# Kernel optimization log

Measured on AMD Instinct MI355X. Metric: run time of the kernel, lower is better.

## Reference

```python
import jax, jax.numpy as jnp
import numpy as np

B, S, D, H, BS = 4, 4096, 1024, 16, 256
DH = D // H  # 64
NB = S // BS  # 16 blocks


def setup_inputs() -> dict:
    key = jax.random.key(0)
    ks = jax.random.split(key, 16)
    sc = 1.0 / np.sqrt(D).astype(np.float32)

    def lin(k):
        return jax.random.normal(k, (D, D), jnp.float32) * sc

    zb = jnp.zeros((D,), jnp.float32)
    return {
        "x": jax.random.normal(ks[0], (B, S, D), jnp.float32),
        "lq_w": lin(ks[1]), "lq_b": zb,
        "lk_w": lin(ks[2]), "lk_b": zb,
        "lv_w": lin(ks[3]), "lv_b": zb,
        "lo_w": lin(ks[4]), "lo_b": zb,
        "pos_bias": jax.random.normal(ks[5], (1, H, BS, BS), jnp.float32) * 0.1,
        "sq_w": lin(ks[6]), "sq_b": zb,
        "sk_w": lin(ks[7]), "sk_b": zb,
        "sv_w": lin(ks[8]), "sv_b": zb,
        "so_w": lin(ks[9]), "so_b": zb,
        "sum_w": lin(ks[10]), "sum_b": zb,
    }


def _mha(x, qw, qb, kw, kb, vw, vb, ow, ob, bias=None):
    # x: [N, L, D] -> multi-head attention, optional additive position bias.
    N, L, _ = x.shape
    q = (x @ qw + qb).reshape(N, L, H, DH).transpose(0, 2, 1, 3)  # [N,H,L,DH]
    k = (x @ kw + kb).reshape(N, L, H, DH).transpose(0, 2, 1, 3)
    v = (x @ vw + vb).reshape(N, L, H, DH).transpose(0, 2, 1, 3)
    scores = jnp.einsum("nhqd,nhkd->nhqk", q, k) / jnp.sqrt(jnp.float32(DH))
    if bias is not None:
        scores = scores + bias[:, :, :L, :L]
    w = jax.nn.softmax(scores, axis=-1)
    ctx = jnp.einsum("nhqk,nhkd->nhqd", w, v)
    ctx = ctx.transpose(0, 2, 1, 3).reshape(N, L, D)
    return ctx @ ow + ob


def reference(x, lq_w, lq_b, lk_w, lk_b, lv_w, lv_b, lo_w, lo_b, pos_bias,
              sq_w, sq_b, sk_w, sk_b, sv_w, sv_b, so_w, so_b, sum_w, sum_b):
    # Local block attention with learned position bias (seq already multiple of BS)
    xb = x.reshape(B * NB, BS, D)
    local = _mha(xb, lq_w, lq_b, lk_w, lk_b, lv_w, lv_b, lo_w, lo_b,
                 bias=pos_bias).reshape(B, S, D)
    # Block summaries: mean-pool each block then linear summarizer
    summaries = x.reshape(B, NB, BS, D).mean(axis=2) @ sum_w + sum_b  # [B,NB,D]
    # Global attention over block summaries (no position bias)
    summ = _mha(summaries, sq_w, sq_b, sk_w, sk_b, sv_w, sv_b, so_w, so_b)
    # Broadcast each block's summary context back to its tokens and combine
    summ_exp = jnp.repeat(summ, BS, axis=1)  # [B,S,D]
    return local + summ_exp
```

## Files before the change

### kernel.cpp

```cpp
#include <hip/hip_runtime.h>
#include <hip/hip_bf16.h>

typedef unsigned short u16;
typedef __bf16 bf16x8 __attribute__((ext_vector_type(8)));
typedef float floatx4 __attribute__((ext_vector_type(4)));
typedef unsigned short u16x4 __attribute__((ext_vector_type(4)));
typedef unsigned short u16x8 __attribute__((ext_vector_type(8)));

__device__ __forceinline__ float b2f(u16 v) {
  unsigned u = ((unsigned)v) << 16;
  return __builtin_bit_cast(float, u);
}
__device__ __forceinline__ u16 f2b(float f) {
  unsigned u = __builtin_bit_cast(unsigned, f);
  unsigned r = (u + 0x7FFFu + ((u >> 16) & 1u)) >> 16;
  return (u16)r;
}
__device__ __forceinline__ void cp16(const u16* g, u16* l) {
  __builtin_amdgcn_global_load_lds(
      (const __attribute__((address_space(1))) unsigned int*)g,
      (__attribute__((address_space(3))) unsigned int*)l, 16, 0, 0);
}

struct GemmArgs {
  const u16* A;
  const u16* BT0; const u16* BT1; const u16* BT2;
  const float* b0; const float* b1; const float* b2;
  const float* summ;
  int srow0;
  u16* C0; u16* C1; u16* C2;
  float* Cf;
};

__global__ __launch_bounds__(256, 2) void gemm_bt(GemmArgs g) {
  const int z = blockIdx.z;
  const u16* A      = g.A;
  const u16* BT     = (z == 0) ? g.BT0 : (z == 1 ? g.BT1 : g.BT2);
  const float* bias = (z == 0) ? g.b0  : (z == 1 ? g.b1  : g.b2);
  u16* C            = (z == 0) ? g.C0  : (z == 1 ? g.C1  : g.C2);

  __shared__ u16 As[128 * 32];
  __shared__ u16 Bs[128 * 32];

  const int tid  = threadIdx.x;
  const int lane = tid & 63;
  const int wave = tid >> 6;
  const int quad = lane >> 4;
  const int cl   = lane & 15;
  const int wm   = wave & 1;
  const int wn   = wave >> 1;

  const size_t row0 = (size_t)blockIdx.x * 128;
  const size_t col0 = (size_t)blockIdx.y * 128;

  const int srow = lane >> 2;
  const int soff = (lane & 3) << 3;

  const u16* gA0 = A + (row0 + (size_t)(wave * 16 + srow)) * 1024 + soff;
  const u16* gA1 = gA0 + (size_t)64 * 1024;
  const u16* gB0 = BT + (col0 + (size_t)(wave * 16 + srow)) * 1024 + soff;
  const u16* gB1 = gB0 + (size_t)64 * 1024;
  u16* lA0 = As + wave * 512 + lane * 8;
  u16* lA1 = lA0 + 2048;
  u16* lB0 = Bs + wave * 512 + lane * 8;
  u16* lB1 = lB0 + 2048;

  floatx4 acc[4][4] = {};

  for (int kt = 0; kt < 1024; kt += 32) {
    __syncthreads();
    cp16(gA0, lA0); cp16(gA1, lA1);
    cp16(gB0, lB0); cp16(gB1, lB1);
    gA0 += 32; gA1 += 32; gB0 += 32; gB1 += 32;
    __syncthreads();
    bf16x8 af[4], bfr[4];
#pragma unroll
    for (int m = 0; m < 4; ++m)
      af[m] = *(const bf16x8*)&As[(wm * 64 + m * 16 + cl) * 32 + quad * 8];
#pragma unroll
    for (int n = 0; n < 4; ++n)
      bfr[n] = *(const bf16x8*)&Bs[(wn * 64 + n * 16 + cl) * 32 + quad * 8];
#pragma unroll
    for (int m = 0; m < 4; ++m)
#pragma unroll
      for (int n = 0; n < 4; ++n)
        acc[m][n] = __builtin_amdgcn_mfma_f32_16x16x32_bf16(af[m], bfr[n],
                                                            acc[m][n], 0, 0, 0);
  }

  const float* summ = g.summ;
#pragma unroll
  for (int m = 0; m < 4; ++m) {
    const size_t rbase = row0 + wm * 64 + m * 16 + quad * 4;
#pragma unroll
    for (int n = 0; n < 4; ++n) {
      const size_t c = col0 + wn * 64 + n * 16 + cl;
      const float bb = bias[c];
#pragma unroll
      for (int e = 0; e < 4; ++e) {
        float v = acc[m][n][e] + bb;
        if (summ)
          v += summ[(size_t)((int)((rbase + e) >> 8) + g.srow0) * 1024 + c];
        if (g.Cf) g.Cf[(rbase + e) * 1024 + c] = v;
        else      C[(rbase + e) * 1024 + c] = f2b(v);
      }
    }
  }
}

__global__ __launch_bounds__(256, 2) void local_attn(
    const u16* __restrict__ Q, const u16* __restrict__ Kt,
    const u16* __restrict__ Vt, const float* __restrict__ pbias,
    u16* __restrict__ ctx) {
  const int qt  = blockIdx.x;
  const int h   = blockIdx.y;
  const int blk = blockIdx.z;
  const int tid  = threadIdx.x;
  const int lane = tid & 63;
  const int w    = tid >> 6;
  const int quad = lane >> 4;
  const int cl   = lane & 15;

  __shared__ u16 BufA[64 * 72];
  __shared__ u16 BufB[64 * 72];

  const size_t tok0  = (size_t)blk * 256;
  const size_t qrow0 = tok0 + qt * 64;
  const int hc = h * 64;

  for (int i = tid; i < 512; i += 256) {
    const int row = i >> 3, c8 = (i & 7) * 8;
    *(u16x8*)&BufA[row * 72 + c8] =
        *(const u16x8*)&Q[(qrow0 + row) * 1024 + hc + c8];
  }

  floatx4 accS[16] = {};
#pragma unroll
  for (int kc = 0; kc < 4; ++kc) {
    __syncthreads();
    for (int i = tid; i < 512; i += 256) {
      const int row = i >> 3, c8 = (i & 7) * 8;
      *(u16x8*)&BufB[row * 72 + c8] =
          *(const u16x8*)&Kt[(tok0 + kc * 64 + row) * 1024 + hc + c8];
    }
    __syncthreads();
#pragma unroll
    for (int ki = 0; ki < 2; ++ki) {
      const bf16x8 aq =
          *(const bf16x8*)&BufA[(w * 16 + cl) * 72 + ki * 32 + quad * 8];
#pragma unroll
      for (int n = 0; n < 4; ++n) {
        const bf16x8 bk =
            *(const bf16x8*)&BufB[(n * 16 + cl) * 72 + ki * 32 + quad * 8];
        accS[kc * 4 + n] = __builtin_amdgcn_mfma_f32_16x16x32_bf16(
            aq, bk, accS[kc * 4 + n], 0, 0, 0);
      }
    }
  }

  float mrow[4] = {-1e30f, -1e30f, -1e30f, -1e30f};
#pragma unroll
  for (int r = 0; r < 4; ++r) {
    const float* brow = pbias + ((size_t)h << 16) +
                        (size_t)(qt * 64 + w * 16 + quad * 4 + r) * 256 + cl;
#pragma unroll
    for (int n = 0; n < 16; ++n) {
      float s = accS[n][r] * 0.125f + brow[n * 16];
      accS[n][r] = s;
      mrow[r] = fmaxf(mrow[r], s);
    }
  }
#pragma unroll
  for (int r = 0; r < 4; ++r) {
#pragma unroll
    for (int st = 1; st < 16; st <<= 1)
      mrow[r] = fmaxf(mrow[r], __shfl_xor(mrow[r], st));
  }
  float lsum[4] = {0.f, 0.f, 0.f, 0.f};
#pragma unroll
  for (int n = 0; n < 16; ++n) {
#pragma unroll
    for (int r = 0; r < 4; ++r) {
      float p = exp2f((accS[n][r] - mrow[r]) * 1.44269504f);
      accS[n][r] = p;
      lsum[r] += p;
    }
  }
#pragma unroll
  for (int r = 0; r < 4; ++r) {
#pragma unroll
    for (int st = 1; st < 16; st <<= 1)
      lsum[r] += __shfl_xor(lsum[r], st);
  }

  floatx4 accO[4] = {};
#pragma unroll
  for (int kc = 0; kc < 4; ++kc) {
    __syncthreads();
#pragma unroll
    for (int nn = 0; nn < 4; ++nn)
#pragma unroll
      for (int r = 0; r < 4; ++r)
        BufA[(w * 16 + quad * 4 + r) * 72 + nn * 16 + cl] =
            f2b(accS[kc * 4 + nn][r]);
    for (int i = tid; i < 512; i += 256) {
      const int key = i & 63, dh0 = (i >> 6) * 8;
      u16x8 v = *(const u16x8*)&Vt[(tok0 + kc * 64 + key) * 1024 + hc + dh0];
#pragma unroll
      for (int j = 0; j < 8; ++j) BufB[(dh0 + j) * 72 + key] = v[j];
    }
    __syncthreads();
#pragma unroll
    for (int ki = 0; ki < 2; ++ki) {
      const bf16x8 ap =
          *(const bf16x8*)&BufA[(w * 16 + cl) * 72 + ki * 32 + quad * 8];
#pragma unroll
      for (int nd = 0; nd < 4; ++nd) {
        const bf16x8 bv =
            *(const bf16x8*)&BufB[(nd * 16 + cl) * 72 + ki * 32 + quad * 8];
        accO[nd] = __builtin_amdgcn_mfma_f32_16x16x32_bf16(ap, bv, accO[nd],
                                                           0, 0, 0);
      }
    }
  }

  float inv[4];
#pragma unroll
  for (int r = 0; r < 4; ++r) inv[r] = 1.0f / lsum[r];
#pragma unroll
  for (int nd = 0; nd < 4; ++nd)
#pragma unroll
    for (int r = 0; r < 4; ++r)
      ctx[(qrow0 + w * 16 + quad * 4 + r) * 1024 + hc + nd * 16 + cl] =
          f2b(accO[nd][r] * inv[r]);
}

__global__ void cvt_x(const float* __restrict__ x, u16* __restrict__ xb) {
  const size_t i = ((size_t)blockIdx.x * 256 + threadIdx.x) * 4;
  float4 v = *(const float4*)&x[i];
  u16x4 o;
  o[0] = f2b(v.x); o[1] = f2b(v.y); o[2] = f2b(v.z); o[3] = f2b(v.w);
  *(u16x4*)&xb[i] = o;
}

__global__ void block_mean(const float* __restrict__ x, u16* __restrict__ xm) {
  const int g = blockIdx.x >> 2;
  const int d = ((blockIdx.x & 3) << 8) + threadIdx.x;
  const float* p = x + (size_t)g * 256 * 1024 + d;
  float s = 0.f;
  for (int t = 0; t < 256; ++t) s += p[(size_t)t * 1024];
  xm[(size_t)g * 1024 + d] = f2b(s * (1.0f / 256.0f));
}

__global__ void summ_attn(const u16* __restrict__ SQ, const u16* __restrict__ SK,
                          const u16* __restrict__ SV, u16* __restrict__ sctx) {
  const int b = blockIdx.x >> 4;
  const int h = blockIdx.x & 15;
  const int t = threadIdx.x;
  __shared__ float Qf[16][64];
  __shared__ float Kf[16][64];
  __shared__ float Vf[16][64];
  __shared__ float sc[16][16];
  for (int i = t; i < 1024; i += 64) {
    const int r = i >> 6, d = i & 63;
    const size_t off = (size_t)(b * 16 + r) * 1024 + h * 64 + d;
    Qf[r][d] = b2f(SQ[off]);
    Kf[r][d] = b2f(SK[off]);
    Vf[r][d] = b2f(SV[off]);
  }
  __syncthreads();
  {
    const int i = t >> 2, j0 = t & 3;
#pragma unroll
    for (int jj = 0; jj < 4; ++jj) {
      const int j = j0 + jj * 4;
      float s = 0.f;
      for (int d = 0; d < 64; ++d) s += Qf[i][d] * Kf[j][d];
      sc[i][j] = s * 0.125f;
    }
  }
  __syncthreads();
  if (t < 16) {
    float m = -1e30f;
    for (int j = 0; j < 16; ++j) m = fmaxf(m, sc[t][j]);
    float l = 0.f;
    for (int j = 0; j < 16; ++j) {
      float p = exp2f((sc[t][j] - m) * 1.44269504f);
      sc[t][j] = p;
      l += p;
    }
    const float inv = 1.0f / l;
    for (int j = 0; j < 16; ++j) sc[t][j] *= inv;
  }
  __syncthreads();
  {
    const int i = t >> 2, d0 = (t & 3) * 16;
    for (int dd = 0; dd < 16; ++dd) {
      float a = 0.f;
      for (int j = 0; j < 16; ++j) a += sc[i][j] * Vf[j][d0 + dd];
      sctx[(size_t)(b * 16 + i) * 1024 + h * 64 + d0 + dd] = f2b(a);
    }
  }
}

struct TPtrs { const float* src[9]; u16* dst[9]; };

__global__ void cvt_transpose9(TPtrs p) {
  const float* src = p.src[blockIdx.z];
  u16* dst         = p.dst[blockIdx.z];
  __shared__ u16 tile[64][72];
  const int r0 = blockIdx.x * 64, c0 = blockIdx.y * 64;
  for (int i = threadIdx.x; i < 1024; i += 256) {
    const int row = i >> 4, c4 = (i & 15) * 4;
    float4 v = *(const float4*)&src[(size_t)(r0 + row) * 1024 + c0 + c4];
    tile[row][c4 + 0] = f2b(v.x);
    tile[row][c4 + 1] = f2b(v.y);
    tile[row][c4 + 2] = f2b(v.z);
    tile[row][c4 + 3] = f2b(v.w);
  }
  __syncthreads();
  for (int i = threadIdx.x; i < 512; i += 256) {
    const int row = i >> 3, c8 = (i & 7) * 8;
    u16x8 v;
#pragma unroll
    for (int j = 0; j < 8; ++j) v[j] = tile[c8 + j][row];
    *(u16x8*)&dst[(size_t)(c0 + row) * 1024 + r0 + c8] = v;
  }
}

extern "C" void kernel_launch(void* const* d_in, const int* in_sizes, int n_in,
                              void* d_out, int out_size, void* d_ws, size_t ws_size,
                              hipStream_t stream) {
  const float* x    = (const float*)d_in[0];
  const float* lqw  = (const float*)d_in[1];
  const float* lqb  = (const float*)d_in[2];
  const float* lkw  = (const float*)d_in[3];
  const float* lkb  = (const float*)d_in[4];
  const float* lvw  = (const float*)d_in[5];
  const float* lvb  = (const float*)d_in[6];
  const float* low_ = (const float*)d_in[7];
  const float* lob  = (const float*)d_in[8];
  const float* pb   = (const float*)d_in[9];
  const float* sqw  = (const float*)d_in[10];
  const float* sqb  = (const float*)d_in[11];
  const float* skw  = (const float*)d_in[12];
  const float* skb  = (const float*)d_in[13];
  const float* svw  = (const float*)d_in[14];
  const float* svb  = (const float*)d_in[15];
  const float* sow  = (const float*)d_in[16];
  const float* sob  = (const float*)d_in[17];
  const float* smw  = (const float*)d_in[18];
  const float* smb  = (const float*)d_in[19];

  char* W = (char*)d_ws;
  size_t off = 0;
  u16* wt[9];
  for (int i = 0; i < 9; ++i) { wt[i] = (u16*)(W + off); off += (size_t)1024 * 1024 * 2; }
  u16* Xb  = (u16*)(W + off); off += (size_t)16384 * 1024 * 2;
  u16* XM  = (u16*)(W + off); off += (size_t)128 * 1024 * 2;
  u16* SMR = (u16*)(W + off); off += (size_t)128 * 1024 * 2;
  u16* SQp = (u16*)(W + off); off += (size_t)128 * 1024 * 2;
  u16* SKp = (u16*)(W + off); off += (size_t)128 * 1024 * 2;
  u16* SVp = (u16*)(W + off); off += (size_t)128 * 1024 * 2;
  u16* SCT = (u16*)(W + off); off += (size_t)128 * 1024 * 2;
  float* SMM = (float*)(W + off); off += (size_t)128 * 1024 * 4;
  const size_t fixedB = off;

  int CH = 256;
  for (int c = 16384; c >= 256; c >>= 1) {
    if (fixedB + (size_t)4 * c * 1024 * 2 <= ws_size) { CH = c; break; }
  }
  u16* Qb  = (u16*)(W + fixedB);
  u16* Kb  = Qb + (size_t)CH * 1024;
  u16* Vb  = Kb + (size_t)CH * 1024;
  u16* CTX = Vb + (size_t)CH * 1024;

  TPtrs tp;
  tp.src[0] = lqw; tp.src[1] = lkw; tp.src[2] = lvw; tp.src[3] = low_;
  tp.src[4] = sqw; tp.src[5] = skw; tp.src[6] = svw; tp.src[7] = sow;
  tp.src[8] = smw;
  for (int i = 0; i < 9; ++i) tp.dst[i] = wt[i];
  cvt_transpose9<<<dim3(16, 16, 9), 256, 0, stream>>>(tp);

  cvt_x<<<dim3(16384), 256, 0, stream>>>(x, Xb);
  block_mean<<<dim3(256), 256, 0, stream>>>(x, XM);

  GemmArgs g1{};
  g1.A = XM; g1.BT0 = g1.BT1 = g1.BT2 = wt[8];
  g1.b0 = g1.b1 = g1.b2 = smb; g1.summ = nullptr; g1.srow0 = 0;
  g1.C0 = g1.C1 = g1.C2 = SMR; g1.Cf = nullptr;
  gemm_bt<<<dim3(1, 8, 1), 256, 0, stream>>>(g1);

  GemmArgs g2{};
  g2.A = SMR; g2.BT0 = wt[4]; g2.BT1 = wt[5]; g2.BT2 = wt[6];
  g2.b0 = sqb; g2.b1 = skb; g2.b2 = svb; g2.summ = nullptr; g2.srow0 = 0;
  g2.C0 = SQp; g2.C1 = SKp; g2.C2 = SVp; g2.Cf = nullptr;
  gemm_bt<<<dim3(1, 8, 3), 256, 0, stream>>>(g2);

  summ_attn<<<dim3(64), 64, 0, stream>>>(SQp, SKp, SVp, SCT);

  GemmArgs g3{};
  g3.A = SCT; g3.BT0 = g3.BT1 = g3.BT2 = wt[7];
  g3.b0 = g3.b1 = g3.b2 = sob; g3.summ = nullptr; g3.srow0 = 0;
  g3.C0 = g3.C1 = g3.C2 = nullptr; g3.Cf = SMM;
  gemm_bt<<<dim3(1, 8, 1), 256, 0, stream>>>(g3);

  for (int base = 0; base < 16384; base += CH) {
    GemmArgs g4{};
    g4.A = Xb + (size_t)base * 1024;
    g4.BT0 = wt[0]; g4.BT1 = wt[1]; g4.BT2 = wt[2];
    g4.b0 = lqb; g4.b1 = lkb; g4.b2 = lvb; g4.summ = nullptr; g4.srow0 = 0;
    g4.C0 = Qb; g4.C1 = Kb; g4.C2 = Vb; g4.Cf = nullptr;
    gemm_bt<<<dim3(CH / 128, 8, 3), 256, 0, stream>>>(g4);

    local_attn<<<dim3(4, 16, CH / 256), 256, 0, stream>>>(Qb, Kb, Vb, pb, CTX);

    GemmArgs g5{};
    g5.A = CTX; g5.BT0 = g5.BT1 = g5.BT2 = wt[3];
    g5.b0 = g5.b1 = g5.b2 = lob; g5.summ = SMM; g5.srow0 = base >> 8;
    g5.C0 = g5.C1 = g5.C2 = nullptr;
    g5.Cf = (float*)d_out + (size_t)base * 1024;
    gemm_bt<<<dim3(CH / 128, 8, 1), 256, 0, stream>>>(g5);
  }

  (void)in_sizes; (void)n_in; (void)out_size;
}
```

Before: 524.7 us.

## Fuse x conversion with block mean, add small GEMM, restructure local attention

Merges the bf16 conversion of x and the per-block mean into one pass, using float atomics into a zeroed buffer, so x is read once instead of twice. Replaces the 128-row tiled GEMM for the 64-row summary projections with a dedicated small GEMM that reads A and weights straight from global memory, taking the fp32 mean directly with the 1/256 scale. Local attention now loads all 256 K rows into LDS at once and keeps Q in registers, then loads a transposed full V tile, which cuts the number of barriers. It also swaps the GEMM grid so consecutive blocks walk columns sharing the same A rows, which may improve L2 reuse. The costs are larger LDS use per block, which may lower occupancy, and atomics whose accumulation order is not fixed.

```diff
diff --git a/kernel.cpp b/kernel.cpp
--- a/kernel.cpp
+++ b/kernel.cpp
@@ -50,8 +50,8 @@
   const int wm   = wave & 1;
   const int wn   = wave >> 1;
 
-  const size_t row0 = (size_t)blockIdx.x * 128;
-  const size_t col0 = (size_t)blockIdx.y * 128;
+  const size_t col0 = (size_t)blockIdx.x * 128;
+  const size_t row0 = (size_t)blockIdx.y * 128;
 
   const int srow = lane >> 2;
   const int soff = (lane & 3) << 3;
@@ -104,6 +104,66 @@
         if (g.Cf) g.Cf[(rbase + e) * 1024 + c] = v;
         else      C[(rbase + e) * 1024 + c] = f2b(v);
       }
+    }
+  }
+}
+
+struct SmallArgs {
+  const void* A;
+  const u16* BT0; const u16* BT1; const u16* BT2;
+  const float* b0; const float* b1; const float* b2;
+  float a_scale; int a_f32;
+  u16* C0; u16* C1; u16* C2;
+  float* Cf;
+};
+
+__global__ __launch_bounds__(256, 2) void small_gemm(SmallArgs s) {
+  const int z = blockIdx.z;
+  const u16* BT     = (z == 0) ? s.BT0 : (z == 1 ? s.BT1 : s.BT2);
+  const float* bias = (z == 0) ? s.b0  : (z == 1 ? s.b1  : s.b2);
+  u16* C            = (z == 0) ? s.C0  : (z == 1 ? s.C1  : s.C2);
+
+  const int tid  = threadIdx.x;
+  const int lane = tid & 63;
+  const int w    = tid >> 6;
+  const int quad = lane >> 4;
+  const int cl   = lane & 15;
+  const int col0 = blockIdx.x * 64;
+  const int arow = w * 16 + cl;
+
+  floatx4 acc[4] = {};
+  for (int k0 = 0; k0 < 1024; k0 += 32) {
+    bf16x8 af;
+    if (s.a_f32) {
+      const float* ap = (const float*)s.A + (size_t)arow * 1024 + k0 + quad * 8;
+      float4 v0 = *(const float4*)ap;
+      float4 v1 = *(const float4*)(ap + 4);
+      u16x8 t;
+      t[0] = f2b(v0.x * s.a_scale); t[1] = f2b(v0.y * s.a_scale);
+      t[2] = f2b(v0.z * s.a_scale); t[3] = f2b(v0.w * s.a_scale);
+      t[4] = f2b(v1.x * s.a_scale); t[5] = f2b(v1.y * s.a_scale);
+      t[6] = f2b(v1.z * s.a_scale); t[7] = f2b(v1.w * s.a_scale);
+      af = __builtin_bit_cast(bf16x8, t);
+    } else {
+      af = *(const bf16x8*)((const u16*)s.A + (size_t)arow * 1024 + k0 + quad * 8);
+    }
+#pragma unroll
+    for (int n = 0; n < 4; ++n) {
+      const bf16x8 bf_ =
+          *(const bf16x8*)&BT[(size_t)(col0 + n * 16 + cl) * 1024 + k0 + quad * 8];
+      acc[n] = __builtin_amdgcn_mfma_f32_16x16x32_bf16(af, bf_, acc[n], 0, 0, 0);
+    }
+  }
+#pragma unroll
+  for (int n = 0; n < 4; ++n) {
+    const int c = col0 + n * 16 + cl;
+    const float bb = bias[c];
+#pragma unroll
+    for (int e = 0; e < 4; ++e) {
+      const int r = w * 16 + quad * 4 + e;
+      const float v = acc[n][e] + bb;
+      if (s.Cf) s.Cf[(size_t)r * 1024 + c] = v;
+      else      C[(size_t)r * 1024 + c] = f2b(v);
     }
   }
 }
@@ -121,41 +181,31 @@
   const int quad = lane >> 4;
   const int cl   = lane & 15;
 
-  __shared__ u16 BufA[64 * 72];
-  __shared__ u16 BufB[64 * 72];
+  __shared__ u16 KV[256 * 72];
+  __shared__ u16 P[64 * 136];
 
   const size_t tok0  = (size_t)blk * 256;
   const size_t qrow0 = tok0 + qt * 64;
   const int hc = h * 64;
 
-  for (int i = tid; i < 512; i += 256) {
+  const u16* qrow = Q + (qrow0 + w * 16 + cl) * 1024 + hc;
+  const bf16x8 aq0 = *(const bf16x8*)&qrow[quad * 8];
+  const bf16x8 aq1 = *(const bf16x8*)&qrow[32 + quad * 8];
+
+  for (int i = tid; i < 2048; i += 256) {
     const int row = i >> 3, c8 = (i & 7) * 8;
-    *(u16x8*)&BufA[row * 72 + c8] =
-        *(const u16x8*)&Q[(qrow0 + row) * 1024 + hc + c8];
-  }
+    *(u16x8*)&KV[row * 72 + c8] =
+        *(const u16x8*)&Kt[(tok0 + row) * 1024 + hc + c8];
+  }
+  __syncthreads();
 
   floatx4 accS[16] = {};
 #pragma unroll
-  for (int kc = 0; kc < 4; ++kc) {
-    __syncthreads();
-    for (int i = tid; i < 512; i += 256) {
-      const int row = i >> 3, c8 = (i & 7) * 8;
-      *(u16x8*)&BufB[row * 72 + c8] =
-          *(const u16x8*)&Kt[(tok0 + kc * 64 + row) * 1024 + hc + c8];
-    }
-    __syncthreads();
-#pragma unroll
-    for (int ki = 0; ki < 2; ++ki) {
-      const bf16x8 aq =
-          *(const bf16x8*)&BufA[(w * 16 + cl) * 72 + ki * 32 + quad * 8];
-#pragma unroll
-      for (int n = 0; n < 4; ++n) {
-        const bf16x8 bk =
-            *(const bf16x8*)&BufB[(n * 16 + cl) * 72 + ki * 32 + quad * 8];
-        accS[kc * 4 + n] = __builtin_amdgcn_mfma_f32_16x16x32_bf16(
-            aq, bk, accS[kc * 4 + n], 0, 0, 0);
-      }
-    }
+  for (int n16 = 0; n16 < 16; ++n16) {
+    const bf16x8 bk0 = *(const bf16x8*)&KV[(n16 * 16 + cl) * 72 + quad * 8];
+    const bf16x8 bk1 = *(const bf16x8*)&KV[(n16 * 16 + cl) * 72 + 32 + quad * 8];
+    accS[n16] = __builtin_amdgcn_mfma_f32_16x16x32_bf16(aq0, bk0, accS[n16], 0, 0, 0);
+    accS[n16] = __builtin_amdgcn_mfma_f32_16x16x32_bf16(aq1, bk1, accS[n16], 0, 0, 0);
   }
 
   float mrow[4] = {-1e30f, -1e30f, -1e30f, -1e30f};
@@ -165,59 +215,57 @@
                         (size_t)(qt * 64 + w * 16 + quad * 4 + r) * 256 + cl;
 #pragma unroll
     for (int n = 0; n < 16; ++n) {
-      float s = accS[n][r] * 0.125f + brow[n * 16];
-      accS[n][r] = s;
-      mrow[r] = fmaxf(mrow[r], s);
-    }
-  }
-#pragma unroll
-  for (int r = 0; r < 4; ++r) {
+      float sv = accS[n][r] * 0.125f + brow[n * 16];
+      accS[n][r] = sv;
+      mrow[r] = fmaxf(mrow[r], sv);
+    }
+  }
+#pragma unroll
+  for (int r = 0; r < 4; ++r)
 #pragma unroll
     for (int st = 1; st < 16; st <<= 1)
       mrow[r] = fmaxf(mrow[r], __shfl_xor(mrow[r], st));
-  }
   float lsum[4] = {0.f, 0.f, 0.f, 0.f};
 #pragma unroll
-  for (int n = 0; n < 16; ++n) {
+  for (int n = 0; n < 16; ++n)
 #pragma unroll
     for (int r = 0; r < 4; ++r) {
       float p = exp2f((accS[n][r] - mrow[r]) * 1.44269504f);
       accS[n][r] = p;
       lsum[r] += p;
     }
-  }
-#pragma unroll
-  for (int r = 0; r < 4; ++r) {
+#pragma unroll
+  for (int r = 0; r < 4; ++r)
 #pragma unroll
     for (int st = 1; st < 16; st <<= 1)
       lsum[r] += __shfl_xor(lsum[r], st);
-  }
+
+  __syncthreads();
+
+  for (int t = 0; t < 8; ++t) {
+    const u16x8 v = *(const u16x8*)&Vt[(tok0 + tid) * 1024 + hc + t * 8];
+#pragma unroll
+    for (int j = 0; j < 8; ++j) KV[(t * 8 + j) * 264 + tid] = v[j];
+  }
+  __syncthreads();
 
   floatx4 accO[4] = {};
 #pragma unroll
-  for (int kc = 0; kc < 4; ++kc) {
-    __syncthreads();
-#pragma unroll
-    for (int nn = 0; nn < 4; ++nn)
+  for (int hf = 0; hf < 2; ++hf) {
+#pragma unroll
+    for (int gi = 0; gi < 8; ++gi)
 #pragma unroll
       for (int r = 0; r < 4; ++r)
-        BufA[(w * 16 + quad * 4 + r) * 72 + nn * 16 + cl] =
-            f2b(accS[kc * 4 + nn][r]);
-    for (int i = tid; i < 512; i += 256) {
-      const int key = i & 63, dh0 = (i >> 6) * 8;
-      u16x8 v = *(const u16x8*)&Vt[(tok0 + kc * 64 + key) * 1024 + hc + dh0];
-#pragma unroll
-      for (int j = 0; j < 8; ++j) BufB[(dh0 + j) * 72 + key] = v[j];
-    }
-    __syncthreads();
-#pragma unroll
-    for (int ki = 0; ki < 2; ++ki) {
+        P[(w * 16 + quad * 4 + r) * 136 + gi * 16 + cl] =
+            f2b(accS[hf * 8 + gi][r]);
+#pragma unroll
+    for (int kk = 0; kk < 4; ++kk) {
       const bf16x8 ap =
-          *(const bf16x8*)&BufA[(w * 16 + cl) * 72 + ki * 32 + quad * 8];
+          *(const bf16x8*)&P[(w * 16 + cl) * 136 + kk * 32 + quad * 8];
 #pragma unroll
       for (int nd = 0; nd < 4; ++nd) {
-        const bf16x8 bv =
-            *(const bf16x8*)&BufB[(nd * 16 + cl) * 72 + ki * 32 + quad * 8];
+        const bf16x8 bv = *(const bf16x8*)&KV[(nd * 16 + cl) * 264 +
+                                              hf * 128 + kk * 32 + quad * 8];
         accO[nd] = __builtin_amdgcn_mfma_f32_16x16x32_bf16(ap, bv, accO[nd],
                                                            0, 0, 0);
       }
@@ -235,21 +283,26 @@
           f2b(accO[nd][r] * inv[r]);
 }
 
-__global__ void cvt_x(const float* __restrict__ x, u16* __restrict__ xb) {
-  const size_t i = ((size_t)blockIdx.x * 256 + threadIdx.x) * 4;
-  float4 v = *(const float4*)&x[i];
-  u16x4 o;
-  o[0] = f2b(v.x); o[1] = f2b(v.y); o[2] = f2b(v.z); o[3] = f2b(v.w);
-  *(u16x4*)&xb[i] = o;
-}
-
-__global__ void block_mean(const float* __restrict__ x, u16* __restrict__ xm) {
-  const int g = blockIdx.x >> 2;
-  const int d = ((blockIdx.x & 3) << 8) + threadIdx.x;
-  const float* p = x + (size_t)g * 256 * 1024 + d;
-  float s = 0.f;
-  for (int t = 0; t < 256; ++t) s += p[(size_t)t * 1024];
-  xm[(size_t)g * 1024 + d] = f2b(s * (1.0f / 256.0f));
+__global__ void cvtx_mean(const float* __restrict__ x, u16* __restrict__ xb,
+                          float* __restrict__ xmf) {
+  const int tq = blockIdx.x;
+  const int g  = blockIdx.y;
+  const int d0 = threadIdx.x * 4;
+  const size_t trow = (size_t)g * 256 + tq * 64;
+  const float* p = x + trow * 1024 + d0;
+  u16* q = xb + trow * 1024 + d0;
+  float4 s = {0.f, 0.f, 0.f, 0.f};
+  for (int t = 0; t < 64; ++t) {
+    float4 v = *(const float4*)(p + (size_t)t * 1024);
+    s.x += v.x; s.y += v.y; s.z += v.z; s.w += v.w;
+    u16x4 o;
+    o[0] = f2b(v.x); o[1] = f2b(v.y); o[2] = f2b(v.z); o[3] = f2b(v.w);
+    *(u16x4*)(q + (size_t)t * 1024) = o;
+  }
+  atomicAdd(&xmf[g * 1024 + d0 + 0], s.x);
+  atomicAdd(&xmf[g * 1024 + d0 + 1], s.y);
+  atomicAdd(&xmf[g * 1024 + d0 + 2], s.z);
+  atomicAdd(&xmf[g * 1024 + d0 + 3], s.w);
 }
 
 __global__ void summ_attn(const u16* __restrict__ SQ, const u16* __restrict__ SK,
@@ -356,14 +409,14 @@
   size_t off = 0;
   u16* wt[9];
   for (int i = 0; i < 9; ++i) { wt[i] = (u16*)(W + off); off += (size_t)1024 * 1024 * 2; }
-  u16* Xb  = (u16*)(W + off); off += (size_t)16384 * 1024 * 2;
-  u16* XM  = (u16*)(W + off); off += (size_t)128 * 1024 * 2;
-  u16* SMR = (u16*)(W + off); off += (size_t)128 * 1024 * 2;
-  u16* SQp = (u16*)(W + off); off += (size_t)128 * 1024 * 2;
-  u16* SKp = (u16*)(W + off); off += (size_t)128 * 1024 * 2;
-  u16* SVp = (u16*)(W + off); off += (size_t)128 * 1024 * 2;
-  u16* SCT = (u16*)(W + off); off += (size_t)128 * 1024 * 2;
-  float* SMM = (float*)(W + off); off += (size_t)128 * 1024 * 4;
+  u16* Xb    = (u16*)(W + off); off += (size_t)16384 * 1024 * 2;
+  float* XMf = (float*)(W + off); off += (size_t)64 * 1024 * 4;
+  u16* SMR   = (u16*)(W + off); off += (size_t)64 * 1024 * 2;
+  u16* SQp   = (u16*)(W + off); off += (size_t)64 * 1024 * 2;
+  u16* SKp   = (u16*)(W + off); off += (size_t)64 * 1024 * 2;
+  u16* SVp   = (u16*)(W + off); off += (size_t)64 * 1024 * 2;
+  u16* SCT   = (u16*)(W + off); off += (size_t)64 * 1024 * 2;
+  float* SMM = (float*)(W + off); off += (size_t)64 * 1024 * 4;
   const size_t fixedB = off;
 
   int CH = 256;
@@ -382,28 +435,31 @@
   for (int i = 0; i < 9; ++i) tp.dst[i] = wt[i];
   cvt_transpose9<<<dim3(16, 16, 9), 256, 0, stream>>>(tp);
 
-  cvt_x<<<dim3(16384), 256, 0, stream>>>(x, Xb);
-  block_mean<<<dim3(256), 256, 0, stream>>>(x, XM);
-
-  GemmArgs g1{};
-  g1.A = XM; g1.BT0 = g1.BT1 = g1.BT2 = wt[8];
-  g1.b0 = g1.b1 = g1.b2 = smb; g1.summ = nullptr; g1.srow0 = 0;
-  g1.C0 = g1.C1 = g1.C2 = SMR; g1.Cf = nullptr;
-  gemm_bt<<<dim3(1, 8, 1), 256, 0, stream>>>(g1);
-
-  GemmArgs g2{};
-  g2.A = SMR; g2.BT0 = wt[4]; g2.BT1 = wt[5]; g2.BT2 = wt[6];
-  g2.b0 = sqb; g2.b1 = skb; g2.b2 = svb; g2.summ = nullptr; g2.srow0 = 0;
-  g2.C0 = SQp; g2.C1 = SKp; g2.C2 = SVp; g2.Cf = nullptr;
-  gemm_bt<<<dim3(1, 8, 3), 256, 0, stream>>>(g2);
+  hipMemsetAsync(XMf, 0, (size_t)64 * 1024 * 4, stream);
+  cvtx_mean<<<dim3(4, 64), 256, 0, stream>>>(x, Xb, XMf);
+
+  SmallArgs s1{};
+  s1.A = XMf; s1.BT0 = s1.BT1 = s1.BT2 = wt[8];
+  s1.b0 = s1.b1 = s1.b2 = smb;
+  s1.a_scale = 1.0f / 256.0f; s1.a_f32 = 1;
+  s1.C0 = s1.C1 = s1.C2 = SMR; s1.Cf = nullptr;
+  small_gemm<<<dim3(16, 1, 1), 256, 0, stream>>>(s1);
+
+  SmallArgs s2{};
+  s2.A = SMR; s2.BT0 = wt[4]; s2.BT1 = wt[5]; s2.BT2 = wt[6];
+  s2.b0 = sqb; s2.b1 = skb; s2.b2 = svb;
+  s2.a_scale = 1.0f; s2.a_f32 = 0;
+  s2.C0 = SQp; s2.C1 = SKp; s2.C2 = SVp; s2.Cf = nullptr;
+  small_gemm<<<dim3(16, 1, 3), 256, 0, stream>>>(s2);
 
   summ_attn<<<dim3(64), 64, 0, stream>>>(SQp, SKp, SVp, SCT);
 
-  GemmArgs g3{};
-  g3.A = SCT; g3.BT0 = g3.BT1 = g3.BT2 = wt[7];
-  g3.b0 = g3.b1 = g3.b2 = sob; g3.summ = nullptr; g3.srow0 = 0;
-  g3.C0 = g3.C1 = g3.C2 = nullptr; g3.Cf = SMM;
-  gemm_bt<<<dim3(1, 8, 1), 256, 0, stream>>>(g3);
+  SmallArgs s3{};
+  s3.A = SCT; s3.BT0 = s3.BT1 = s3.BT2 = wt[7];
+  s3.b0 = s3.b1 = s3.b2 = sob;
+  s3.a_scale = 1.0f; s3.a_f32 = 0;
+  s3.C0 = s3.C1 = s3.C2 = nullptr; s3.Cf = SMM;
+  small_gemm<<<dim3(16, 1, 1), 256, 0, stream>>>(s3);
 
   for (int base = 0; base < 16384; base += CH) {
     GemmArgs g4{};
@@ -411,7 +467,7 @@
     g4.BT0 = wt[0]; g4.BT1 = wt[1]; g4.BT2 = wt[2];
     g4.b0 = lqb; g4.b1 = lkb; g4.b2 = lvb; g4.summ = nullptr; g4.srow0 = 0;
     g4.C0 = Qb; g4.C1 = Kb; g4.C2 = Vb; g4.Cf = nullptr;
-    gemm_bt<<<dim3(CH / 128, 8, 3), 256, 0, stream>>>(g4);
+    gemm_bt<<<dim3(8, CH / 128, 3), 256, 0, stream>>>(g4);
 
     local_attn<<<dim3(4, 16, CH / 256), 256, 0, stream>>>(Qb, Kb, Vb, pb, CTX);
 
@@ -420,7 +476,7 @@
     g5.b0 = g5.b1 = g5.b2 = lob; g5.summ = SMM; g5.srow0 = base >> 8;
     g5.C0 = g5.C1 = g5.C2 = nullptr;
     g5.Cf = (float*)d_out + (size_t)base * 1024;
-    gemm_bt<<<dim3(CH / 128, 8, 1), 256, 0, stream>>>(g5);
+    gemm_bt<<<dim3(8, CH / 128, 1), 256, 0, stream>>>(g5);
   }
 
   (void)in_sizes; (void)n_in; (void)out_size;
```

After: 556.9 us. 6.1% more time.
